# Performance work log

Measured on AMD Instinct MI355X. Metric: run time of the kernel, lower is better.

## Reference

```python
import jax, jax.numpy as jnp
import numpy as np

P, L, H = 8192, 64, 128
EPS = 1e-5


def _layer(x, W, b, g, be):
    # Linear -> LayerNorm (last dim) -> ReLU, applied to every (polyline, vector) slot.
    y = x @ W + b
    mu = jnp.mean(y, axis=-1, keepdims=True)
    var = jnp.mean((y - mu) ** 2, axis=-1, keepdims=True)
    y = (y - mu) / jnp.sqrt(var + EPS) * g + be
    return jax.nn.relu(y)


def _agg_cat(x, mask):
    # masked max over the vector dim, broadcast back and concat (the 'repeat + cat' in torch)
    phi = jnp.max(jnp.where(mask[..., None], x, -jnp.inf), axis=1, keepdims=True)  # (P,1,H)
    return jnp.concatenate([x, jnp.broadcast_to(phi, x.shape)], axis=-1)  # (P,L,2H)


def setup_inputs() -> dict:
    key = jax.random.key(0)
    ks = jax.random.split(key, 16)
    hidden_states = jax.random.normal(ks[0], (P, L, H), dtype=jnp.float32)
    lengths = jnp.maximum(jax.random.randint(ks[1], (P,), 0, L + 1), 1).astype(jnp.int32)
    s1 = 1.0 / np.sqrt(H)
    s2 = 1.0 / np.sqrt(2 * H)
    return {
        "hidden_states": hidden_states,
        "lengths": lengths,
        "W1": jax.random.normal(ks[2], (H, H), dtype=jnp.float32) * s1,
        "b1": jnp.zeros((H,), jnp.float32),
        "g1": jnp.ones((H,), jnp.float32),
        "be1": jnp.zeros((H,), jnp.float32),
        "W2": jax.random.normal(ks[3], (2 * H, H), dtype=jnp.float32) * s2,
        "b2": jnp.zeros((H,), jnp.float32),
        "g2": jnp.ones((H,), jnp.float32),
        "be2": jnp.zeros((H,), jnp.float32),
        "W3": jax.random.normal(ks[4], (2 * H, H), dtype=jnp.float32) * s2,
        "b3": jnp.zeros((H,), jnp.float32),
        "g3": jnp.ones((H,), jnp.float32),
        "be3": jnp.zeros((H,), jnp.float32),
    }


def reference(hidden_states, lengths, W1, b1, g1, be1, W2, b2, g2, be2, W3, b3, g3, be3):
    mask = jnp.arange(L)[None, :] < lengths[:, None]  # (P,L) valid-vector mask
    x = _layer(hidden_states, W1, b1, g1, be1)
    out = _agg_cat(x, mask)
    x = _layer(out, W2, b2, g2, be2)
    out = _agg_cat(x, mask)
    x = _layer(out, W3, b3, g3, be3)
    out = _agg_cat(x, mask)
    # final masked max-pool over vectors -> (P, 2H)
    poly_features = jnp.max(jnp.where(mask[..., None], out, -jnp.inf), axis=1)
    return poly_features
```

## Files before the change

kernel.cpp:

```cpp
#include <hip/hip_runtime.h>
#include <stdint.h>

#define PCNT 8192
#define LROW 64
#define HDIM 128
#define XSTR 136
#define WBUF_ELEMS (128 * XSTR)

typedef _Float16 f16;
typedef __attribute__((ext_vector_type(8))) _Float16 half8;
typedef __attribute__((ext_vector_type(4))) _Float16 half4v;
typedef __attribute__((ext_vector_type(2))) _Float16 half2v;
typedef __attribute__((ext_vector_type(4))) float f32x4;

#define MFMA16(A, B, C) __builtin_amdgcn_mfma_f32_16x16x32_f16((A), (B), (C), 0, 0, 0)

__device__ __forceinline__ half8 ldh8(const f16* p) {
  return *reinterpret_cast<const half8*>(p);
}

union PkU { uint32_t u; half2v h; };

__device__ __forceinline__ uint32_t pk2(float lo, float hi) {
  PkU a;
  a.h[0] = (f16)lo;
  a.h[1] = (f16)hi;
  return a.u;
}

__device__ __forceinline__ uint32_t pkmax(uint32_t a, uint32_t b) {
  uint32_t d;
  asm("v_pk_max_f16 %0, %1, %2" : "=v"(d) : "v"(a), "v"(b));
  return d;
}

__global__ void prep_weights(const float* __restrict__ W1,
                             const float* __restrict__ W2,
                             const float* __restrict__ W3,
                             f16* __restrict__ wt) {
  int idx = blockIdx.x * 256 + threadIdx.x;
  if (idx >= 5 * WBUF_ELEMS) return;
  int buf = idx / WBUF_ELEMS;
  int rem = idx - buf * WBUF_ELEMS;
  int c = rem / XSTR;
  int k = rem - c * XSTR;
  float v = 0.0f;
  if (k < 128) {
    const float* W = (buf == 0) ? W1 : (buf <= 2 ? W2 : W3);
    int krow = k + ((buf == 2 || buf == 4) ? 128 : 0);
    v = W[krow * 128 + c];
  }
  wt[idx] = (f16)v;
}

__global__ __launch_bounds__(256, 6)
void fused_subgraph(const float* __restrict__ hs,
                    const int* __restrict__ lens,
                    const f16* __restrict__ wt,
                    const float* __restrict__ b1, const float* __restrict__ g1, const float* __restrict__ be1,
                    const float* __restrict__ b2, const float* __restrict__ g2, const float* __restrict__ be2,
                    const float* __restrict__ b3, const float* __restrict__ g3, const float* __restrict__ be3,
                    float* __restrict__ out) {
  __shared__ __align__(16) f16 x_lds[LROW * XSTR];
  __shared__ float2 stats_s[4][LROW];
  __shared__ __align__(16) f16 phib[HDIM];

  const int tid = threadIdx.x;
  const int w = tid >> 6;
  const int l = tid & 63;
  const int p = blockIdx.x;

  int len = lens[p];
  len = (len < 1) ? 1 : (len > LROW ? LROW : len);
  const int mtiles = (len + 15) >> 4;

  const int l15 = l & 15;
  const int lg = l >> 4;
  const int ko = lg * 8;
  const int cb0 = w * 32 + lg * 4;
  const int cb1 = cb0 + 16;
  const int wrow0 = (w * 32 + l15) * XSTR;
  const int wrow1 = (w * 32 + 16 + l15) * XSTR;

  {
    const float* hp = hs + (size_t)p * (LROW * HDIM);
    for (int it = 0; it < mtiles; ++it) {
      int e = (it * 256 + tid) * 8;
      int r = e >> 7, c = e & 127;
      float4 va = *reinterpret_cast<const float4*>(hp + e);
      float4 vb = *reinterpret_cast<const float4*>(hp + e + 4);
      half8 hv;
      hv[0] = (f16)va.x; hv[1] = (f16)va.y; hv[2] = (f16)va.z; hv[3] = (f16)va.w;
      hv[4] = (f16)vb.x; hv[5] = (f16)vb.y; hv[6] = (f16)vb.z; hv[7] = (f16)vb.w;
      *reinterpret_cast<half8*>(&x_lds[r * XSTR + c]) = hv;
    }
  }
  __syncthreads();

#pragma unroll
  for (int layer = 0; layer < 3; ++layer) {
    const float* gv  = (layer == 0) ? g1  : (layer == 1) ? g2  : g3;
    const float* bev = (layer == 0) ? be1 : (layer == 1) ? be2 : be3;
    const float* bv  = (layer == 0) ? b1  : (layer == 1) ? b2  : b3;
    const f16* wa = wt + (size_t)((layer == 0) ? 0 : (layer == 1) ? 1 : 3) * WBUF_ELEMS;

    f32x4 pva0, pva1;
    {
      const float4 bl0 = *reinterpret_cast<const float4*>(bv + cb0);
      const float4 bl1 = *reinterpret_cast<const float4*>(bv + cb1);
      pva0[0] = bl0.x; pva0[1] = bl0.y; pva0[2] = bl0.z; pva0[3] = bl0.w;
      pva1[0] = bl1.x; pva1[1] = bl1.y; pva1[2] = bl1.z; pva1[3] = bl1.w;
    }
    if (layer > 0) {
      const f16* wb = wt + (size_t)((layer == 1) ? 2 : 4) * WBUF_ELEMS;
#pragma unroll
      for (int kc = 0; kc < 4; ++kc) {
        half8 wb0 = ldh8(&wb[wrow0 + kc * 32 + ko]);
        half8 wb1 = ldh8(&wb[wrow1 + kc * 32 + ko]);
        half8 ph = ldh8(&phib[kc * 32 + ko]);
        pva0 = MFMA16(wb0, ph, pva0);
        pva1 = MFMA16(wb1, ph, pva1);
      }
    }

    f32x4 acc[4][2];
#pragma unroll
    for (int mt = 0; mt < 4; ++mt) { acc[mt][0] = pva0; acc[mt][1] = pva1; }
#pragma unroll
    for (int kc = 0; kc < 4; ++kc) {
      half8 wa0 = ldh8(&wa[wrow0 + kc * 32 + ko]);
      half8 wa1 = ldh8(&wa[wrow1 + kc * 32 + ko]);
#pragma unroll
      for (int mt = 0; mt < 4; ++mt) {
        if (mt < mtiles) {
          half8 bx = ldh8(&x_lds[(mt * 16 + l15) * XSTR + kc * 32 + ko]);
          acc[mt][0] = MFMA16(wa0, bx, acc[mt][0]);
          acc[mt][1] = MFMA16(wa1, bx, acc[mt][1]);
        }
      }
    }

#pragma unroll
    for (int mt = 0; mt < 4; ++mt) {
      if (mt < mtiles) {
        const f32x4 a0 = acc[mt][0], a1 = acc[mt][1];
        float s = ((a0[0] + a0[1]) + (a0[2] + a0[3])) + ((a1[0] + a1[1]) + (a1[2] + a1[3]));
        float q = a0[0] * a0[0];
        q = fmaf(a0[1], a0[1], q); q = fmaf(a0[2], a0[2], q); q = fmaf(a0[3], a0[3], q);
        q = fmaf(a1[0], a1[0], q); q = fmaf(a1[1], a1[1], q);
        q = fmaf(a1[2], a1[2], q); q = fmaf(a1[3], a1[3], q);
        s += __shfl_xor(s, 16); q += __shfl_xor(q, 16);
        s += __shfl_xor(s, 32); q += __shfl_xor(q, 32);
        if (l < 16) stats_s[w][mt * 16 + l15] = make_float2(s, q);
      }
    }
    __syncthreads();

    const float4 gg0 = *reinterpret_cast<const float4*>(gv + cb0);
    const float4 gg1 = *reinterpret_cast<const float4*>(gv + cb1);
    const float4 eb0 = *reinterpret_cast<const float4*>(bev + cb0);
    const float4 eb1 = *reinterpret_cast<const float4*>(bev + cb1);
    uint32_t pm[4] = {0u, 0u, 0u, 0u};
#pragma unroll
    for (int mt = 0; mt < 4; ++mt) {
      if (mt < mtiles) {
        const int row = mt * 16 + l15;
        float2 t0 = stats_s[0][row], t1 = stats_s[1][row];
        float2 t2 = stats_s[2][row], t3 = stats_s[3][row];
        float s = (t0.x + t1.x) + (t2.x + t3.x);
        float q = (t0.y + t1.y) + (t2.y + t3.y);
        float mu = s * (1.0f / 128.0f);
        float var = q * (1.0f / 128.0f) - mu * mu;
        float rs = rsqrtf(var + 1e-5f);
        const bool valid = row < len;
        float v0 = fmaxf((acc[mt][0][0] - mu) * rs * gg0.x + eb0.x, 0.0f);
        float v1 = fmaxf((acc[mt][0][1] - mu) * rs * gg0.y + eb0.y, 0.0f);
        float v2 = fmaxf((acc[mt][0][2] - mu) * rs * gg0.z + eb0.z, 0.0f);
        float v3 = fmaxf((acc[mt][0][3] - mu) * rs * gg0.w + eb0.w, 0.0f);
        float u0 = fmaxf((acc[mt][1][0] - mu) * rs * gg1.x + eb1.x, 0.0f);
        float u1 = fmaxf((acc[mt][1][1] - mu) * rs * gg1.y + eb1.y, 0.0f);
        float u2 = fmaxf((acc[mt][1][2] - mu) * rs * gg1.z + eb1.z, 0.0f);
        float u3 = fmaxf((acc[mt][1][3] - mu) * rs * gg1.w + eb1.w, 0.0f);
        if (layer < 2) {
          half4v h0; h0[0] = (f16)v0; h0[1] = (f16)v1; h0[2] = (f16)v2; h0[3] = (f16)v3;
          half4v h1; h1[0] = (f16)u0; h1[1] = (f16)u1; h1[2] = (f16)u2; h1[3] = (f16)u3;
          *reinterpret_cast<half4v*>(&x_lds[row * XSTR + cb0]) = h0;
          *reinterpret_cast<half4v*>(&x_lds[row * XSTR + cb1]) = h1;
        }
        pm[0] = pkmax(pm[0], pk2(valid ? v0 : 0.0f, valid ? v1 : 0.0f));
        pm[1] = pkmax(pm[1], pk2(valid ? v2 : 0.0f, valid ? v3 : 0.0f));
        pm[2] = pkmax(pm[2], pk2(valid ? u0 : 0.0f, valid ? u1 : 0.0f));
        pm[3] = pkmax(pm[3], pk2(valid ? u2 : 0.0f, valid ? u3 : 0.0f));
      }
    }
#pragma unroll
    for (int d = 1; d <= 8; d <<= 1) {
#pragma unroll
      for (int j = 0; j < 4; ++j)
        pm[j] = pkmax(pm[j], (uint32_t)__shfl_xor((int)pm[j], d));
    }

    if (layer < 2) {
      if (l15 == 0) {
        *reinterpret_cast<uint2*>(&phib[cb0]) = make_uint2(pm[0], pm[1]);
        *reinterpret_cast<uint2*>(&phib[cb1]) = make_uint2(pm[2], pm[3]);
      }
      __syncthreads();
    } else {
      if (l15 == 0) {
        PkU q0, q1, q2, q3;
        q0.u = pm[0]; q1.u = pm[1]; q2.u = pm[2]; q3.u = pm[3];
        float4 o0 = make_float4((float)q0.h[0], (float)q0.h[1], (float)q1.h[0], (float)q1.h[1]);
        float4 o1 = make_float4((float)q2.h[0], (float)q2.h[1], (float)q3.h[0], (float)q3.h[1]);
        float* op = out + (size_t)p * 256;
        *reinterpret_cast<float4*>(op + cb0) = o0;
        *reinterpret_cast<float4*>(op + cb1) = o1;
        *reinterpret_cast<float4*>(op + 128 + cb0) = o0;
        *reinterpret_cast<float4*>(op + 128 + cb1) = o1;
      }
    }
  }
}

extern "C" void kernel_launch(void* const* d_in, const int* in_sizes, int n_in,
                              void* d_out, int out_size, void* d_ws, size_t ws_size,
                              hipStream_t stream) {
  const float* hs  = (const float*)d_in[0];
  const int* lens  = (const int*)d_in[1];
  const float* W1  = (const float*)d_in[2];
  const float* b1  = (const float*)d_in[3];
  const float* g1  = (const float*)d_in[4];
  const float* be1 = (const float*)d_in[5];
  const float* W2  = (const float*)d_in[6];
  const float* b2  = (const float*)d_in[7];
  const float* g2  = (const float*)d_in[8];
  const float* be2 = (const float*)d_in[9];
  const float* W3  = (const float*)d_in[10];
  const float* b3  = (const float*)d_in[11];
  const float* g3  = (const float*)d_in[12];
  const float* be3 = (const float*)d_in[13];
  float* out = (float*)d_out;
  f16* wt = (f16*)d_ws;

  const int prep_total = 5 * WBUF_ELEMS;
  prep_weights<<<(prep_total + 255) / 256, 256, 0, stream>>>(W1, W2, W3, wt);
  fused_subgraph<<<PCNT, 256, 0, stream>>>(hs, lens, wt,
                                           b1, g1, be1, b2, g2, be2, b3, g3, be3,
                                           out);
}
```

Baseline: 134.0 us.

## Merge phi projection into main K loop with wider interleaved weight layout

Weights for layers 2 and 3 are now stored as a single 256-wide K row per output column instead of two separate 128-wide buffers. The main MFMA loop runs up to 8 K-chunks, and the last 4 multiply the broadcast phi vector into every row tile. Before, phi was projected once and used as the accumulator's starting value. This removes the separate pre-pass but adds redundant MFMAs per m-tile. Stats LDS is transposed so each row's four partials come in two float4 loads, and launch bounds drop from 6 to 4 blocks per CU, which changes register and occupancy tradeoffs.

```diff
diff --git a/kernel.cpp b/kernel.cpp
--- a/kernel.cpp
+++ b/kernel.cpp
@@ -5,7 +5,10 @@
 #define LROW 64
 #define HDIM 128
 #define XSTR 136
-#define WBUF_ELEMS (128 * XSTR)
+#define W1STR 136
+#define W23STR 264
+#define W1_ELEMS (128 * W1STR)
+#define W23_ELEMS (128 * W23STR)
 
 typedef _Float16 f16;
 typedef __attribute__((ext_vector_type(8))) _Float16 half8;
@@ -39,21 +42,22 @@
                              const float* __restrict__ W3,
                              f16* __restrict__ wt) {
   int idx = blockIdx.x * 256 + threadIdx.x;
-  if (idx >= 5 * WBUF_ELEMS) return;
-  int buf = idx / WBUF_ELEMS;
-  int rem = idx - buf * WBUF_ELEMS;
-  int c = rem / XSTR;
-  int k = rem - c * XSTR;
+  if (idx >= W1_ELEMS + 2 * W23_ELEMS) return;
   float v = 0.0f;
-  if (k < 128) {
-    const float* W = (buf == 0) ? W1 : (buf <= 2 ? W2 : W3);
-    int krow = k + ((buf == 2 || buf == 4) ? 128 : 0);
-    v = W[krow * 128 + c];
+  if (idx < W1_ELEMS) {
+    int c = idx / W1STR, k = idx - c * W1STR;
+    if (k < 128) v = W1[k * 128 + c];
+  } else {
+    int rem = idx - W1_ELEMS;
+    const float* W = (rem < W23_ELEMS) ? W2 : W3;
+    if (rem >= W23_ELEMS) rem -= W23_ELEMS;
+    int c = rem / W23STR, k = rem - c * W23STR;
+    if (k < 256) v = W[k * 128 + c];
   }
   wt[idx] = (f16)v;
 }
 
-__global__ __launch_bounds__(256, 6)
+__global__ __launch_bounds__(256, 4)
 void fused_subgraph(const float* __restrict__ hs,
                     const int* __restrict__ lens,
                     const f16* __restrict__ wt,
@@ -62,7 +66,7 @@
                     const float* __restrict__ b3, const float* __restrict__ g3, const float* __restrict__ be3,
                     float* __restrict__ out) {
   __shared__ __align__(16) f16 x_lds[LROW * XSTR];
-  __shared__ float2 stats_s[4][LROW];
+  __shared__ __align__(16) float2 stats_s[LROW][4];
   __shared__ __align__(16) f16 phib[HDIM];
 
   const int tid = threadIdx.x;
@@ -79,8 +83,6 @@
   const int ko = lg * 8;
   const int cb0 = w * 32 + lg * 4;
   const int cb1 = cb0 + 16;
-  const int wrow0 = (w * 32 + l15) * XSTR;
-  const int wrow1 = (w * 32 + 16 + l15) * XSTR;
 
   {
     const float* hp = hs + (size_t)p * (LROW * HDIM);
@@ -102,40 +104,46 @@
     const float* gv  = (layer == 0) ? g1  : (layer == 1) ? g2  : g3;
     const float* bev = (layer == 0) ? be1 : (layer == 1) ? be2 : be3;
     const float* bv  = (layer == 0) ? b1  : (layer == 1) ? b2  : b3;
-    const f16* wa = wt + (size_t)((layer == 0) ? 0 : (layer == 1) ? 1 : 3) * WBUF_ELEMS;
-
-    f32x4 pva0, pva1;
+    const f16* wa = (layer == 0) ? wt
+                   : (layer == 1) ? (wt + W1_ELEMS)
+                                  : (wt + W1_ELEMS + W23_ELEMS);
+    const int wstr = (layer == 0) ? W1STR : W23STR;
+    const int kcN  = (layer == 0) ? 4 : 8;
+    const int wrow0 = (w * 32 + l15) * wstr;
+    const int wrow1 = wrow0 + 16 * wstr;
+
+    f32x4 acc[4][2];
     {
       const float4 bl0 = *reinterpret_cast<const float4*>(bv + cb0);
       const float4 bl1 = *reinterpret_cast<const float4*>(bv + cb1);
-      pva0[0] = bl0.x; pva0[1] = bl0.y; pva0[2] = bl0.z; pva0[3] = bl0.w;
-      pva1[0] = bl1.x; pva1[1] = bl1.y; pva1[2] = bl1.z; pva1[3] = bl1.w;
-    }
-    if (layer > 0) {
-      const f16* wb = wt + (size_t)((layer == 1) ? 2 : 4) * WBUF_ELEMS;
-#pragma unroll
-      for (int kc = 0; kc < 4; ++kc) {
-        half8 wb0 = ldh8(&wb[wrow0 + kc * 32 + ko]);
-        half8 wb1 = ldh8(&wb[wrow1 + kc * 32 + ko]);
-        half8 ph = ldh8(&phib[kc * 32 + ko]);
-        pva0 = MFMA16(wb0, ph, pva0);
-        pva1 = MFMA16(wb1, ph, pva1);
-      }
-    }
-
-    f32x4 acc[4][2];
-#pragma unroll
-    for (int mt = 0; mt < 4; ++mt) { acc[mt][0] = pva0; acc[mt][1] = pva1; }
-#pragma unroll
-    for (int kc = 0; kc < 4; ++kc) {
+      f32x4 s0, s1;
+      s0[0] = bl0.x; s0[1] = bl0.y; s0[2] = bl0.z; s0[3] = bl0.w;
+      s1[0] = bl1.x; s1[1] = bl1.y; s1[2] = bl1.z; s1[3] = bl1.w;
+#pragma unroll
+      for (int mt = 0; mt < 4; ++mt) { acc[mt][0] = s0; acc[mt][1] = s1; }
+    }
+#pragma unroll
+    for (int kc = 0; kc < 8; ++kc) {
+      if (kc >= kcN) break;
       half8 wa0 = ldh8(&wa[wrow0 + kc * 32 + ko]);
       half8 wa1 = ldh8(&wa[wrow1 + kc * 32 + ko]);
-#pragma unroll
-      for (int mt = 0; mt < 4; ++mt) {
-        if (mt < mtiles) {
-          half8 bx = ldh8(&x_lds[(mt * 16 + l15) * XSTR + kc * 32 + ko]);
-          acc[mt][0] = MFMA16(wa0, bx, acc[mt][0]);
-          acc[mt][1] = MFMA16(wa1, bx, acc[mt][1]);
+      if (kc < 4) {
+#pragma unroll
+        for (int mt = 0; mt < 4; ++mt) {
+          if (mt < mtiles) {
+            half8 bx = ldh8(&x_lds[(mt * 16 + l15) * XSTR + kc * 32 + ko]);
+            acc[mt][0] = MFMA16(wa0, bx, acc[mt][0]);
+            acc[mt][1] = MFMA16(wa1, bx, acc[mt][1]);
+          }
+        }
+      } else {
+        half8 ph = ldh8(&phib[(kc - 4) * 32 + ko]);
+#pragma unroll
+        for (int mt = 0; mt < 4; ++mt) {
+          if (mt < mtiles) {
+            acc[mt][0] = MFMA16(wa0, ph, acc[mt][0]);
+            acc[mt][1] = MFMA16(wa1, ph, acc[mt][1]);
+          }
         }
       }
     }
@@ -151,7 +159,7 @@
         q = fmaf(a1[2], a1[2], q); q = fmaf(a1[3], a1[3], q);
         s += __shfl_xor(s, 16); q += __shfl_xor(q, 16);
         s += __shfl_xor(s, 32); q += __shfl_xor(q, 32);
-        if (l < 16) stats_s[w][mt * 16 + l15] = make_float2(s, q);
+        if (l < 16) stats_s[mt * 16 + l15][w] = make_float2(s, q);
       }
     }
     __syncthreads();
@@ -165,10 +173,10 @@
     for (int mt = 0; mt < 4; ++mt) {
       if (mt < mtiles) {
         const int row = mt * 16 + l15;
-        float2 t0 = stats_s[0][row], t1 = stats_s[1][row];
-        float2 t2 = stats_s[2][row], t3 = stats_s[3][row];
-        float s = (t0.x + t1.x) + (t2.x + t3.x);
-        float q = (t0.y + t1.y) + (t2.y + t3.y);
+        float4 r01 = *reinterpret_cast<const float4*>(&stats_s[row][0]);
+        float4 r23 = *reinterpret_cast<const float4*>(&stats_s[row][2]);
+        float s = (r01.x + r01.z) + (r23.x + r23.z);
+        float q = (r01.y + r01.w) + (r23.y + r23.w);
         float mu = s * (1.0f / 128.0f);
         float var = q * (1.0f / 128.0f) - mu * mu;
         float rs = rsqrtf(var + 1e-5f);
@@ -242,7 +250,7 @@
   float* out = (float*)d_out;
   f16* wt = (f16*)d_ws;
 
-  const int prep_total = 5 * WBUF_ELEMS;
+  const int prep_total = W1_ELEMS + 2 * W23_ELEMS;
   prep_weights<<<(prep_total + 255) / 256, 256, 0, stream>>>(W1, W2, W3, wt);
   fused_subgraph<<<PCNT, 256, 0, stream>>>(hs, lens, wt,
                                            b1, g1, be1, b2, g2, be2, b3, g3, be3,
```

Measured after the change: 134.3 us. Within noise of the previous version (+0.3%).
